# Kernel optimization log

Measured on AMD Instinct MI355X. Metric: run time of the kernel, lower is better.

Reference implementation:

```python
import jax, jax.numpy as jnp
import numpy as np

B, N, C, H = 2, 2048, 768, 12
HD = C // H  # head dim = 64


def setup_inputs() -> dict:
    key = jax.random.key(0)
    k1, k2, k3 = jax.random.split(key, 3)
    x = jax.random.normal(k1, (B, N, C), dtype=jnp.float32)
    w_qkv = jax.random.normal(k2, (C, 3 * C), dtype=jnp.float32) * (C ** -0.5)
    w_proj = jax.random.normal(k3, (C, C), dtype=jnp.float32) * (C ** -0.5)
    b_proj = jnp.zeros((C,), dtype=jnp.float32)
    return {"x": x, "w_qkv": w_qkv, "w_proj": w_proj, "b_proj": b_proj}


def reference(x, w_qkv, w_proj, b_proj):
    scale = HD ** -0.5
    # qkv projection: [B,N,3C] -> [3,B,H,N,HD]
    qkv = (x @ w_qkv).reshape(B, N, 3, H, HD).transpose(2, 0, 3, 1, 4)
    q, k, v = qkv[0], qkv[1], qkv[2]
    # explicit QK^T softmax V (materializes [B,H,N,N] scores, as in source)
    attn = jnp.einsum("bhqd,bhkd->bhqk", q, k) * scale
    attn = jax.nn.softmax(attn, axis=-1)
    out = jnp.einsum("bhqk,bhkd->bhqd", attn, v)
    out = out.transpose(0, 2, 1, 3).reshape(B, N, C)
    return out @ w_proj + b_proj
```

## Files before the change

### kernel.cpp

```cpp
#include <hip/hip_runtime.h>

#define C_DIM 768
#define NSEQ 2048
#define H_DIM 12
#define HD 64
#define M_ROWS 4096

typedef float f32x4 __attribute__((ext_vector_type(4)));
typedef short bf16x8 __attribute__((ext_vector_type(8)));
typedef _Float16 f16x8 __attribute__((ext_vector_type(8)));
typedef _Float16 f16x4 __attribute__((ext_vector_type(4)));
typedef __fp16 fp16x2 __attribute__((ext_vector_type(2)));
typedef unsigned short u16;

#define MFMA_PV(a, b, c) __builtin_amdgcn_mfma_f32_16x16x16f16(a, b, c, 0, 0, 0)

typedef unsigned int __attribute__((address_space(1))) as1_uint;
typedef unsigned int __attribute__((address_space(3))) as3_uint;
__device__ __forceinline__ void dma16(const void* g, void* l) {
  __builtin_amdgcn_global_load_lds((const as1_uint*)g, (as3_uint*)l, 16, 0, 0);
}

__device__ __forceinline__ u16 f2bf(float f) {
  union { float f; unsigned u; } v; v.f = f;
  unsigned u = v.u + 0x7FFFu + ((v.u >> 16) & 1u);
  return (u16)(u >> 16);
}

__global__ __launch_bounds__(256) void cvt_x_kernel(const float* __restrict__ in,
                                                    u16* __restrict__ out, int n4) {
  int i = blockIdx.x * 256 + threadIdx.x;
  if (i < n4) {
    float4 v = ((const float4*)in)[i];
    ushort4 o;
    o.x = f2bf(v.x); o.y = f2bf(v.y); o.z = f2bf(v.z); o.w = f2bf(v.w);
    ((ushort4*)out)[i] = o;
  }
}

__global__ __launch_bounds__(256) void transpose_cvt_kernel(const float* __restrict__ wq,
                                                            const float* __restrict__ wp,
                                                            u16* __restrict__ outq,
                                                            u16* __restrict__ outp) {
  const float* in; u16* out; int Cc;
  if (blockIdx.z == 0) { in = wq; out = outq; Cc = 3 * C_DIM; }
  else { if (blockIdx.x >= 24) return; in = wp; out = outp; Cc = C_DIM; }
  const int R = C_DIM;
  __shared__ float t[32][33];
  int tx = threadIdx.x & 31, ty = threadIdx.x >> 5;
  int c0 = blockIdx.x * 32, r0 = blockIdx.y * 32;
#pragma unroll
  for (int i = 0; i < 4; i++)
    t[ty + i * 8][tx] = in[(size_t)(r0 + ty + i * 8) * Cc + c0 + tx];
  __syncthreads();
#pragma unroll
  for (int i = 0; i < 4; i++)
    out[(size_t)(c0 + ty + i * 8) * R + r0 + tx] = f2bf(t[tx][ty + i * 8]);
}

__device__ __forceinline__ void gemm_core_128(const u16* __restrict__ A,
                                              const u16* __restrict__ BT,
                                              int m0, int n0,
                                              u16* la, u16* lb, f32x4 acc[4][4]) {
  const int K = C_DIM;
  int tid = threadIdx.x, lane = tid & 63, wave = tid >> 6;
  int wm = (wave >> 1) * 64, wn = (wave & 1) * 64;
  int quad = lane >> 4, l16 = lane & 15;

  int r0 = wave * 16 + (lane >> 2);
  int sw = (((lane & 3) ^ (r0 & 3)) * 8);
  const u16* ga0 = A + (size_t)(m0 + r0) * K + sw;
  const u16* ga1 = A + (size_t)(m0 + r0 + 64) * K + sw;
  const u16* gb0 = BT + (size_t)(n0 + r0) * K + sw;
  const u16* gb1 = BT + (size_t)(n0 + r0 + 64) * K + sw;
  u16* lA0 = la + wave * 16 * 32;
  u16* lA1 = lA0 + 64 * 32;
  u16* lB0 = lb + wave * 16 * 32;
  u16* lB1 = lB0 + 64 * 32;

  for (int k0 = 0; k0 < K; k0 += 32) {
    __syncthreads();
    dma16(ga0 + k0, lA0);
    dma16(ga1 + k0, lA1);
    dma16(gb0 + k0, lB0);
    dma16(gb1 + k0, lB1);
    __syncthreads();
    bf16x8 af[4], bfr[4];
#pragma unroll
    for (int mt = 0; mt < 4; mt++) {
      int r = wm + mt * 16 + l16;
      af[mt] = *(const bf16x8*)(la + r * 32 + ((quad ^ (r & 3)) * 8));
    }
#pragma unroll
    for (int nt = 0; nt < 4; nt++) {
      int r = wn + nt * 16 + l16;
      bfr[nt] = *(const bf16x8*)(lb + r * 32 + ((quad ^ (r & 3)) * 8));
    }
#pragma unroll
    for (int mt = 0; mt < 4; mt++)
#pragma unroll
      for (int nt = 0; nt < 4; nt++)
        acc[mt][nt] = __builtin_amdgcn_mfma_f32_16x16x32_bf16(af[mt], bfr[nt], acc[mt][nt], 0, 0, 0);
  }
}

__device__ __forceinline__ void gemm_core_64(const u16* __restrict__ A,
                                             const u16* __restrict__ BT,
                                             int m0, int n0,
                                             u16* la, u16* lb, f32x4 acc[2][4]) {
  const int K = C_DIM;
  int tid = threadIdx.x, lane = tid & 63, wave = tid >> 6;
  int wm = (wave >> 1) * 32, wn = (wave & 1) * 64;
  int quad = lane >> 4, l16 = lane & 15;

  int r0 = wave * 16 + (lane >> 2);
  int sw = (((lane & 3) ^ (r0 & 3)) * 8);
  const u16* ga0 = A + (size_t)(m0 + r0) * K + sw;
  const u16* gb0 = BT + (size_t)(n0 + r0) * K + sw;
  const u16* gb1 = BT + (size_t)(n0 + r0 + 64) * K + sw;
  u16* lA0 = la + wave * 16 * 32;
  u16* lB0 = lb + wave * 16 * 32;
  u16* lB1 = lB0 + 64 * 32;

  for (int k0 = 0; k0 < K; k0 += 32) {
    __syncthreads();
    dma16(ga0 + k0, lA0);
    dma16(gb0 + k0, lB0);
    dma16(gb1 + k0, lB1);
    __syncthreads();
    bf16x8 af[2], bfr[4];
#pragma unroll
    for (int mt = 0; mt < 2; mt++) {
      int r = wm + mt * 16 + l16;
      af[mt] = *(const bf16x8*)(la + r * 32 + ((quad ^ (r & 3)) * 8));
    }
#pragma unroll
    for (int nt = 0; nt < 4; nt++) {
      int r = wn + nt * 16 + l16;
      bfr[nt] = *(const bf16x8*)(lb + r * 32 + ((quad ^ (r & 3)) * 8));
    }
#pragma unroll
    for (int mt = 0; mt < 2; mt++)
#pragma unroll
      for (int nt = 0; nt < 4; nt++)
        acc[mt][nt] = __builtin_amdgcn_mfma_f32_16x16x32_bf16(af[mt], bfr[nt], acc[mt][nt], 0, 0, 0);
  }
}

#define Q_PRESCALE 0.18033688011112042f
__global__ __launch_bounds__(256) void gemm_qkv_kernel(const u16* __restrict__ A,
                                                       const u16* __restrict__ BT,
                                                       _Float16* __restrict__ qb,
                                                       _Float16* __restrict__ kb,
                                                       _Float16* __restrict__ vtb) {
  __shared__ __align__(16) u16 la[128 * 32];
  __shared__ __align__(16) u16 lb[128 * 32];
  f32x4 acc[4][4] = {};
  int m0 = blockIdx.x * 128, n0 = blockIdx.y * 128;
  gemm_core_128(A, BT, m0, n0, la, lb, acc);

  int lane = threadIdx.x & 63, wave = threadIdx.x >> 6;
  int wm = (wave >> 1) * 64, wn = (wave & 1) * 64;
  int quad = lane >> 4, l16 = lane & 15;
#pragma unroll
  for (int mt = 0; mt < 4; mt++) {
#pragma unroll
    for (int nt = 0; nt < 4; nt++) {
      int gn = n0 + wn + nt * 16 + l16;
      int which = gn / C_DIM;
      int cc = gn - which * C_DIM;
      int h = cc >> 6, d = cc & 63;
      int gm0 = m0 + wm + mt * 16 + quad * 4;
      int b = gm0 >> 11, n = gm0 & 2047;
      size_t bh = (size_t)(b * H_DIM + h);
      if (which == 2) {
        f16x4 hv;
#pragma unroll
        for (int r = 0; r < 4; r++) hv[r] = (_Float16)acc[mt][nt][r];
        *(f16x4*)(vtb + (bh * HD + d) * NSEQ + n) = hv;
      } else if (which == 0) {
#pragma unroll
        for (int r = 0; r < 4; r++)
          qb[(bh * NSEQ + n + r) * HD + d] = (_Float16)(acc[mt][nt][r] * Q_PRESCALE);
      } else {
#pragma unroll
        for (int r = 0; r < 4; r++)
          kb[(bh * NSEQ + n + r) * HD + d] = (_Float16)acc[mt][nt][r];
      }
    }
  }
}

__global__ __launch_bounds__(256) void gemm_proj_kernel(const u16* __restrict__ A,
                                                        const u16* __restrict__ BT,
                                                        const float* __restrict__ bias,
                                                        float* __restrict__ out) {
  __shared__ __align__(16) u16 la[64 * 32];
  __shared__ __align__(16) u16 lb[128 * 32];
  f32x4 acc[2][4] = {};
  int m0 = blockIdx.x * 64, n0 = blockIdx.y * 128;
  gemm_core_64(A, BT, m0, n0, la, lb, acc);

  int lane = threadIdx.x & 63, wave = threadIdx.x >> 6;
  int wm = (wave >> 1) * 32, wn = (wave & 1) * 64;
  int quad = lane >> 4, l16 = lane & 15;
#pragma unroll
  for (int mt = 0; mt < 2; mt++) {
#pragma unroll
    for (int nt = 0; nt < 4; nt++) {
      int gn = n0 + wn + nt * 16 + l16;
      float bv = bias[gn];
#pragma unroll
      for (int r = 0; r < 4; r++) {
        int gm = m0 + wm + mt * 16 + quad * 4 + r;
        out[(size_t)gm * C_DIM + gn] = acc[mt][nt][r] + bv;
      }
    }
  }
}

__global__ __launch_bounds__(128) void attn_kernel(const _Float16* __restrict__ qb,
                                                   const _Float16* __restrict__ kb,
                                                   const _Float16* __restrict__ vtb,
                                                   u16* __restrict__ attn) {
  __shared__ __align__(16) u16 lk[2][64 * 64];
  __shared__ __align__(16) u16 lv[2][64 * 64];
  int bh = blockIdx.y, qblk = blockIdx.x;
  int tid = threadIdx.x, lane = tid & 63, wave = tid >> 6;
  int quad = lane >> 4, l16 = lane & 15;

  const _Float16* q_bh = qb + (size_t)bh * NSEQ * HD;
  const u16* k_bh = (const u16*)(kb + (size_t)bh * NSEQ * HD);
  const u16* v_bh = (const u16*)(vtb + (size_t)bh * HD * NSEQ);

  int q0 = qblk * 64 + wave * 32 + l16;
  f16x8 qf[2][2];
#pragma unroll
  for (int qt = 0; qt < 2; qt++) {
    const _Float16* qp = q_bh + (size_t)(q0 + qt * 16) * HD + quad * 8;
    qf[qt][0] = *(const f16x8*)qp;
    qf[qt][1] = *(const f16x8*)(qp + 32);
  }

  f32x4 o[2][4] = {};
  float l_i[2] = {0.f, 0.f};

  int sr = wave * 32 + (lane >> 3);
  int sw = (((lane & 7) ^ (sr & 7)) * 8);
  const u16* gk = k_bh + (size_t)sr * HD + sw;
  const u16* gv = v_bh + (size_t)sr * NSEQ + sw;
  int lbase = wave * 32 * 64;

#define STAGE_KV(buf, kk)                                            \
  {                                                                  \
    _Pragma("unroll") for (int j = 0; j < 4; j++) {                  \
      dma16(gk + (size_t)((kk) + j * 8) * HD, &lk[buf][lbase + j * 512]); \
      dma16(gv + (size_t)(j * 8) * NSEQ + (kk), &lv[buf][lbase + j * 512]); \
    }                                                                \
  }

  STAGE_KV(0, 0);

  for (int kt = 0; kt < 32; kt++) {
    int cur = kt & 1;
    __syncthreads();
    if (kt < 31) STAGE_KV(cur ^ 1, (kt + 1) * 64);

    f32x4 s0[4], s1[4];
#pragma unroll
    for (int nt = 0; nt < 4; nt++) {
      const u16* kbp = lk[cur] + (nt * 16 + l16) * 64;
      int rs = l16 & 7;
      f16x8 kf0 = *(const f16x8*)(kbp + ((quad ^ rs) * 8));
      f16x8 kf1 = *(const f16x8*)(kbp + (((quad + 4) ^ rs) * 8));
      f32x4 t0 = {}, t1 = {};
      t0 = __builtin_amdgcn_mfma_f32_16x16x32_f16(kf0, qf[0][0], t0, 0, 0, 0);
      t0 = __builtin_amdgcn_mfma_f32_16x16x32_f16(kf1, qf[0][1], t0, 0, 0, 0);
      t1 = __builtin_amdgcn_mfma_f32_16x16x32_f16(kf0, qf[1][0], t1, 0, 0, 0);
      t1 = __builtin_amdgcn_mfma_f32_16x16x32_f16(kf1, qf[1][1], t1, 0, 0, 0);
      s0[nt] = t0; s1[nt] = t1;
    }

#pragma unroll
    for (int nt = 0; nt < 4; nt++) {
      float a0 = __builtin_amdgcn_exp2f(s0[nt][0]);
      float a1 = __builtin_amdgcn_exp2f(s0[nt][1]);
      float a2 = __builtin_amdgcn_exp2f(s0[nt][2]);
      float a3 = __builtin_amdgcn_exp2f(s0[nt][3]);
      l_i[0] += (a0 + a1) + (a2 + a3);
      float b0 = __builtin_amdgcn_exp2f(s1[nt][0]);
      float b1 = __builtin_amdgcn_exp2f(s1[nt][1]);
      float b2 = __builtin_amdgcn_exp2f(s1[nt][2]);
      float b3 = __builtin_amdgcn_exp2f(s1[nt][3]);
      l_i[1] += (b0 + b1) + (b2 + b3);
      union { fp16x2 h2[2]; f16x4 h4; } pa, pb;
      pa.h2[0] = __builtin_amdgcn_cvt_pkrtz(a0, a1);
      pa.h2[1] = __builtin_amdgcn_cvt_pkrtz(a2, a3);
      pb.h2[0] = __builtin_amdgcn_cvt_pkrtz(b0, b1);
      pb.h2[1] = __builtin_amdgcn_cvt_pkrtz(b2, b3);
#pragma unroll
      for (int dt = 0; dt < 4; dt++) {
        int r = dt * 16 + l16;
        int c = nt * 2 + (quad >> 1);
        f16x4 vf = *(const f16x4*)(lv[cur] + r * 64 + ((c ^ (l16 & 7)) * 8) + (quad & 1) * 4);
        o[0][dt] = MFMA_PV(vf, pa.h4, o[0][dt]);
        o[1][dt] = MFMA_PV(vf, pb.h4, o[1][dt]);
      }
    }
  }

#pragma unroll
  for (int qt = 0; qt < 2; qt++) {
    l_i[qt] += __shfl_xor(l_i[qt], 16);
    l_i[qt] += __shfl_xor(l_i[qt], 32);
  }

  int b = bh / H_DIM, h = bh % H_DIM;
#pragma unroll
  for (int qt = 0; qt < 2; qt++) {
    float inv = 1.f / l_i[qt];
    int q = q0 + qt * 16;
    u16* orow = attn + (size_t)(b * NSEQ + q) * C_DIM + h * HD;
#pragma unroll
    for (int dt = 0; dt < 4; dt++) {
      ushort4 ov;
      ov.x = f2bf(o[qt][dt][0] * inv);
      ov.y = f2bf(o[qt][dt][1] * inv);
      ov.z = f2bf(o[qt][dt][2] * inv);
      ov.w = f2bf(o[qt][dt][3] * inv);
      *(ushort4*)(orow + dt * 16 + quad * 4) = ov;
    }
  }
}

extern "C" void kernel_launch(void* const* d_in, const int* in_sizes, int n_in,
                              void* d_out, int out_size, void* d_ws, size_t ws_size,
                              hipStream_t stream) {
  const float* x = (const float*)d_in[0];
  const float* w_qkv = (const float*)d_in[1];
  const float* w_proj = (const float*)d_in[2];
  const float* b_proj = (const float*)d_in[3];
  float* out = (float*)d_out;

  char* ws = (char*)d_ws;
  u16* x_bf        = (u16*)(ws);
  u16* wqkvT       = (u16*)(ws + 6291456);
  u16* wprojT      = (u16*)(ws + 9830400);
  _Float16* qb     = (_Float16*)(ws + 11010048);
  _Float16* kb     = (_Float16*)(ws + 17301504);
  _Float16* vtb    = (_Float16*)(ws + 23592960);
  u16* attn        = x_bf;

  cvt_x_kernel<<<3072, 256, 0, stream>>>(x, x_bf, M_ROWS * C_DIM / 4);
  transpose_cvt_kernel<<<dim3(72, 24, 2), 256, 0, stream>>>(w_qkv, w_proj, wqkvT, wprojT);
  gemm_qkv_kernel<<<dim3(32, 18), 256, 0, stream>>>(x_bf, wqkvT, qb, kb, vtb);
  attn_kernel<<<dim3(32, 24), 128, 0, stream>>>(qb, kb, vtb, attn);
  gemm_proj_kernel<<<dim3(64, 6), 256, 0, stream>>>(attn, wprojT, b_proj, out);
}
```

Baseline: 174.2 us.

## Split attention over key range with partial outputs and a combine kernel

```diff
diff --git a/kernel.cpp b/kernel.cpp
--- a/kernel.cpp
+++ b/kernel.cpp
@@ -5,12 +5,14 @@
 #define H_DIM 12
 #define HD 64
 #define M_ROWS 4096
+#define KSPLIT 2
 
 typedef float f32x4 __attribute__((ext_vector_type(4)));
 typedef short bf16x8 __attribute__((ext_vector_type(8)));
 typedef _Float16 f16x8 __attribute__((ext_vector_type(8)));
 typedef _Float16 f16x4 __attribute__((ext_vector_type(4)));
 typedef __fp16 fp16x2 __attribute__((ext_vector_type(2)));
+typedef __fp16 fp16x4 __attribute__((ext_vector_type(4)));
 typedef unsigned short u16;
 
 #define MFMA_PV(a, b, c) __builtin_amdgcn_mfma_f32_16x16x16f16(a, b, c, 0, 0, 0)
@@ -219,13 +221,14 @@
   }
 }
 
-__global__ __launch_bounds__(128) void attn_kernel(const _Float16* __restrict__ qb,
+__global__ __launch_bounds__(256) void attn_kernel(const _Float16* __restrict__ qb,
                                                    const _Float16* __restrict__ kb,
                                                    const _Float16* __restrict__ vtb,
-                                                   u16* __restrict__ attn) {
-  __shared__ __align__(16) u16 lk[2][64 * 64];
-  __shared__ __align__(16) u16 lv[2][64 * 64];
-  int bh = blockIdx.y, qblk = blockIdx.x;
+                                                   __fp16* __restrict__ opart,
+                                                   float* __restrict__ lpart) {
+  __shared__ __align__(16) u16 lk[2][64 * 72];
+  __shared__ __align__(16) u16 lv[2][64 * 72];
+  int bh = blockIdx.y, qblk = blockIdx.x, ks = blockIdx.z;
   int tid = threadIdx.x, lane = tid & 63, wave = tid >> 6;
   int quad = lane >> 4, l16 = lane & 15;
 
@@ -233,7 +236,7 @@
   const u16* k_bh = (const u16*)(kb + (size_t)bh * NSEQ * HD);
   const u16* v_bh = (const u16*)(vtb + (size_t)bh * HD * NSEQ);
 
-  int q0 = qblk * 64 + wave * 32 + l16;
+  int q0 = qblk * 128 + wave * 32 + l16;
   f16x8 qf[2][2];
 #pragma unroll
   for (int qt = 0; qt < 2; qt++) {
@@ -245,34 +248,43 @@
   f32x4 o[2][4] = {};
   float l_i[2] = {0.f, 0.f};
 
-  int sr = wave * 32 + (lane >> 3);
-  int sw = (((lane & 7) ^ (sr & 7)) * 8);
-  const u16* gk = k_bh + (size_t)sr * HD + sw;
-  const u16* gv = v_bh + (size_t)sr * NSEQ + sw;
-  int lbase = wave * 32 * 64;
-
-#define STAGE_KV(buf, kk)                                            \
-  {                                                                  \
-    _Pragma("unroll") for (int j = 0; j < 4; j++) {                  \
-      dma16(gk + (size_t)((kk) + j * 8) * HD, &lk[buf][lbase + j * 512]); \
-      dma16(gv + (size_t)(j * 8) * NSEQ + (kk), &lv[buf][lbase + j * 512]); \
-    }                                                                \
-  }
-
-  STAGE_KV(0, 0);
-
-  for (int kt = 0; kt < 32; kt++) {
-    int cur = kt & 1;
+  int srow = tid >> 3, scj = tid & 7;
+  const u16* kp0 = k_bh + (size_t)srow * HD + scj * 8;
+  const u16* kp1 = kp0 + (size_t)32 * HD;
+  const u16* vp0 = v_bh + (size_t)srow * NSEQ + scj * 8;
+  const u16* vp1 = vp0 + (size_t)32 * NSEQ;
+  int w0 = srow * 72 + scj * 8, w1 = (srow + 32) * 72 + scj * 8;
+
+  const int kt_beg = ks * (NSEQ / 64 / KSPLIT);
+  const int kt_end = kt_beg + (NSEQ / 64 / KSPLIT);
+
+  {
+    int k0 = kt_beg * 64;
+    *(uint4*)(lk[0] + w0) = *(const uint4*)(kp0 + (size_t)k0 * HD);
+    *(uint4*)(lk[0] + w1) = *(const uint4*)(kp1 + (size_t)k0 * HD);
+    *(uint4*)(lv[0] + w0) = *(const uint4*)(vp0 + k0);
+    *(uint4*)(lv[0] + w1) = *(const uint4*)(vp1 + k0);
+  }
+
+  for (int kt = kt_beg; kt < kt_end; kt++) {
+    int cur = kt & 1, nxt = cur ^ 1;
     __syncthreads();
-    if (kt < 31) STAGE_KV(cur ^ 1, (kt + 1) * 64);
+
+    uint4 rk0, rk1, rv0, rv1;
+    if (kt < kt_end - 1) {
+      int k0 = (kt + 1) * 64;
+      rk0 = *(const uint4*)(kp0 + (size_t)k0 * HD);
+      rk1 = *(const uint4*)(kp1 + (size_t)k0 * HD);
+      rv0 = *(const uint4*)(vp0 + k0);
+      rv1 = *(const uint4*)(vp1 + k0);
+    }
 
     f32x4 s0[4], s1[4];
 #pragma unroll
     for (int nt = 0; nt < 4; nt++) {
-      const u16* kbp = lk[cur] + (nt * 16 + l16) * 64;
-      int rs = l16 & 7;
-      f16x8 kf0 = *(const f16x8*)(kbp + ((quad ^ rs) * 8));
-      f16x8 kf1 = *(const f16x8*)(kbp + (((quad + 4) ^ rs) * 8));
+      const u16* kp = lk[cur] + (nt * 16 + l16) * 72 + quad * 8;
+      f16x8 kf0 = *(const f16x8*)kp;
+      f16x8 kf1 = *(const f16x8*)(kp + 32);
       f32x4 t0 = {}, t1 = {};
       t0 = __builtin_amdgcn_mfma_f32_16x16x32_f16(kf0, qf[0][0], t0, 0, 0, 0);
       t0 = __builtin_amdgcn_mfma_f32_16x16x32_f16(kf1, qf[0][1], t0, 0, 0, 0);
@@ -300,13 +312,18 @@
       pb.h2[1] = __builtin_amdgcn_cvt_pkrtz(b2, b3);
 #pragma unroll
       for (int dt = 0; dt < 4; dt++) {
-        int r = dt * 16 + l16;
-        int c = nt * 2 + (quad >> 1);
-        f16x4 vf = *(const f16x4*)(lv[cur] + r * 64 + ((c ^ (l16 & 7)) * 8) + (quad & 1) * 4);
+        f16x4 vf = *(const f16x4*)(lv[cur] + (dt * 16 + l16) * 72 + nt * 16 + quad * 4);
         o[0][dt] = MFMA_PV(vf, pa.h4, o[0][dt]);
         o[1][dt] = MFMA_PV(vf, pb.h4, o[1][dt]);
       }
     }
+
+    if (kt < kt_end - 1) {
+      *(uint4*)(lk[nxt] + w0) = rk0;
+      *(uint4*)(lk[nxt] + w1) = rk1;
+      *(uint4*)(lv[nxt] + w0) = rv0;
+      *(uint4*)(lv[nxt] + w1) = rv1;
+    }
   }
 
 #pragma unroll
@@ -316,21 +333,52 @@
   }
 
   int b = bh / H_DIM, h = bh % H_DIM;
+  __fp16* obase = opart + (size_t)ks * M_ROWS * C_DIM;
+  float* lrow = lpart + ((size_t)ks * H_DIM * 2 + bh) * NSEQ;
 #pragma unroll
   for (int qt = 0; qt < 2; qt++) {
-    float inv = 1.f / l_i[qt];
     int q = q0 + qt * 16;
-    u16* orow = attn + (size_t)(b * NSEQ + q) * C_DIM + h * HD;
+    if (quad == 0) lrow[q] = l_i[qt];
+    __fp16* orow = obase + (size_t)(b * NSEQ + q) * C_DIM + h * HD;
 #pragma unroll
     for (int dt = 0; dt < 4; dt++) {
-      ushort4 ov;
-      ov.x = f2bf(o[qt][dt][0] * inv);
-      ov.y = f2bf(o[qt][dt][1] * inv);
-      ov.z = f2bf(o[qt][dt][2] * inv);
-      ov.w = f2bf(o[qt][dt][3] * inv);
-      *(ushort4*)(orow + dt * 16 + quad * 4) = ov;
-    }
-  }
+      union { fp16x2 h2[2]; fp16x4 h4; } ov;
+      ov.h2[0] = __builtin_amdgcn_cvt_pkrtz(o[qt][dt][0], o[qt][dt][1]);
+      ov.h2[1] = __builtin_amdgcn_cvt_pkrtz(o[qt][dt][2], o[qt][dt][3]);
+      *(fp16x4*)(orow + dt * 16 + quad * 4) = ov.h4;
+    }
+  }
+}
+
+__global__ __launch_bounds__(256) void combine_kernel(const __fp16* __restrict__ opart,
+                                                      const float* __restrict__ lpart,
+                                                      u16* __restrict__ attn) {
+  int idx = blockIdx.x * 256 + threadIdx.x;
+  int bq = idx / (C_DIM / 8);
+  int c = (idx - bq * (C_DIM / 8)) * 8;
+  int h = c >> 6;
+  int b = bq >> 11, q = bq & 2047;
+  size_t lidx = (size_t)(b * H_DIM + h) * NSEQ + q;
+  float l = lpart[lidx] + lpart[lidx + (size_t)H_DIM * 2 * NSEQ];
+  float inv = 1.f / l;
+  const __fp16* p0 = opart + (size_t)bq * C_DIM + c;
+  const __fp16* p1 = p0 + (size_t)M_ROWS * C_DIM;
+  fp16x4 a0 = *(const fp16x4*)p0, a1 = *(const fp16x4*)(p0 + 4);
+  fp16x4 b0 = *(const fp16x4*)p1, b1 = *(const fp16x4*)(p1 + 4);
+  union { ushort4 s4[2]; uint4 u4; } ov;
+#pragma unroll
+  for (int j = 0; j < 4; j++) {
+    ov.s4[0].x = f2bf(((float)a0[0] + (float)b0[0]) * inv);
+  }
+  ov.s4[0].x = f2bf(((float)a0[0] + (float)b0[0]) * inv);
+  ov.s4[0].y = f2bf(((float)a0[1] + (float)b0[1]) * inv);
+  ov.s4[0].z = f2bf(((float)a0[2] + (float)b0[2]) * inv);
+  ov.s4[0].w = f2bf(((float)a0[3] + (float)b0[3]) * inv);
+  ov.s4[1].x = f2bf(((float)a1[0] + (float)b1[0]) * inv);
+  ov.s4[1].y = f2bf(((float)a1[1] + (float)b1[1]) * inv);
+  ov.s4[1].z = f2bf(((float)a1[2] + (float)b1[2]) * inv);
+  ov.s4[1].w = f2bf(((float)a1[3] + (float)b1[3]) * inv);
+  *(uint4*)(attn + (size_t)bq * C_DIM + c) = ov.u4;
 }
 
 extern "C" void kernel_launch(void* const* d_in, const int* in_sizes, int n_in,
@@ -349,11 +397,14 @@
   _Float16* qb     = (_Float16*)(ws + 11010048);
   _Float16* kb     = (_Float16*)(ws + 17301504);
   _Float16* vtb    = (_Float16*)(ws + 23592960);
+  __fp16* opart    = (__fp16*)(ws + 29884416);
+  float* lpart     = (float*)(ws + 42467328);
   u16* attn        = x_bf;
 
   cvt_x_kernel<<<3072, 256, 0, stream>>>(x, x_bf, M_ROWS * C_DIM / 4);
   transpose_cvt_kernel<<<dim3(72, 24, 2), 256, 0, stream>>>(w_qkv, w_proj, wqkvT, wprojT);
   gemm_qkv_kernel<<<dim3(32, 18), 256, 0, stream>>>(x_bf, wqkvT, qb, kb, vtb);
-  attn_kernel<<<dim3(32, 24), 128, 0, stream>>>(qb, kb, vtb, attn);
+  attn_kernel<<<dim3(16, 24, KSPLIT), 256, 0, stream>>>(qb, kb, vtb, opart, lpart);
+  combine_kernel<<<M_ROWS * C_DIM / 8 / 256, 256, 0, stream>>>(opart, lpart, attn);
   gemm_proj_kernel<<<dim3(64, 6), 256, 0, stream>>>(attn, wprojT, b_proj, out);
 }
```

Result: faster. 159.9 us (-8.2%).
